# Kernel tuning notes

Measured on AMD Instinct MI355X. Metric: run time of the kernel, lower is better.

The kernel has to match this reference:

```python
import jax, jax.numpy as jnp
import numpy as np

B, N, D, H = 8, 1024, 512, 8
DH = D // H


def setup_inputs() -> dict:
    key = jax.random.key(0)
    ks = jax.random.split(key, 7)
    s = 1.0 / np.sqrt(D)
    return {
        "x": jax.random.normal(ks[0], (B, N, D), dtype=jnp.float32),
        "Wq": jax.random.normal(ks[1], (D, D), dtype=jnp.float32) * s,
        "bq": jax.random.normal(ks[2], (D,), dtype=jnp.float32) * 0.01,
        "Wk": jax.random.normal(ks[3], (D, D), dtype=jnp.float32) * s,
        "bk": jax.random.normal(ks[4], (D,), dtype=jnp.float32) * 0.01,
        "Wv": jax.random.normal(ks[5], (D, D), dtype=jnp.float32) * s,
        "bv": jax.random.normal(ks[6], (D,), dtype=jnp.float32) * 0.01,
    }


def reference(x, Wq, bq, Wk, bk, Wv, bv):
    # Q/K/V projections (nn.Linear: x @ W^T + b; here W stored as [in, out])
    q = x @ Wq + bq  # [B, N, D]
    k = x @ Wk + bk
    v = x @ Wv + bv
    # chunk(dim=2)+cat(dim=0) == split channels into H head groups
    q = q.reshape(B, N, H, DH)
    k = k.reshape(B, N, H, DH)
    v = v.reshape(B, N, H, DH)
    # NOTE: original applies NO 1/sqrt(head_dim) scaling
    scores = jnp.einsum("bqhd,bkhd->bhqk", q, k)  # [B, H, N, N]
    weights = jax.nn.softmax(scores, axis=-1)
    y = jnp.einsum("bhqk,bkhd->bqhd", weights, v)  # [B, N, H, DH]
    return y.reshape(B, N, D)
```

## Files before the change

kernel.cpp:

```cpp
#include <hip/hip_runtime.h>
#include <hip/hip_bf16.h>

typedef _Float16 half8 __attribute__((ext_vector_type(8)));
typedef _Float16 half4v __attribute__((ext_vector_type(4)));
typedef float floatx4 __attribute__((ext_vector_type(4)));

#define BB 8
#define NN 1024
#define DD 512
#define HH 8
#define DHH 64
#define LOG2E 1.4426950408889634f

#define EXP2F(x) __builtin_amdgcn_exp2f(x)

__device__ __forceinline__ void gload_lds16(const _Float16* g, _Float16* l) {
    __builtin_amdgcn_global_load_lds(
        (const __attribute__((address_space(1))) void*)g,
        (__attribute__((address_space(3))) void*)l, 16, 0, 0);
}

__global__ __launch_bounds__(256) void cvt_kernel(const float* __restrict__ Wq,
                                                  const float* __restrict__ Wk,
                                                  const float* __restrict__ Wv,
                                                  _Float16* __restrict__ Wt) {
    __shared__ __align__(16) _Float16 tb[64][72];
    int t = blockIdx.x;
    int tid = threadIdx.x;
    int which = t >> 6;
    int rem = t & 63;
    int kt = (rem >> 3) * 64, nt = (rem & 7) * 64;
    const float* W = (which == 0) ? Wq : (which == 1) ? Wk : Wv;
    float wscale = (which == 0) ? LOG2E : 1.0f;
    _Float16* Wto = Wt + (size_t)which * DD * DD;
    for (int i = 0; i < 16; i++) {
        int idx = tid + i * 256;
        int r = idx >> 6, c = idx & 63;
        tb[c][r] = (_Float16)(W[(size_t)(kt + r) * DD + nt + c] * wscale);
    }
    __syncthreads();
    for (int i = 0; i < 16; i++) {
        int idx = tid + i * 256;
        int r = idx >> 6, c = idx & 63;
        Wto[(size_t)(nt + r) * DD + kt + c] = tb[r][c];
    }
}

__global__ __launch_bounds__(256) void qkv_gemm_kernel(const float* __restrict__ x,
                                                       const _Float16* __restrict__ Wt,
                                                       const float* __restrict__ bq,
                                                       const float* __restrict__ bk,
                                                       const float* __restrict__ bv,
                                                       _Float16* __restrict__ QKV) {
    __shared__ __align__(16) _Float16 Ws[128 * 32];
    __shared__ __align__(16) _Float16 Xs[128 * 32];

    int which = blockIdx.z;
    const _Float16* Wtw = Wt + (size_t)which * DD * DD;
    const float* bias = (which == 0) ? bq : (which == 1) ? bk : bv;
    const float bscale = (which == 0) ? LOG2E : 1.0f;

    int tid = threadIdx.x;
    int wave = tid >> 6, lane = tid & 63;
    int quad = lane >> 4, l16 = lane & 15;
    int wm = wave >> 1, wn = wave & 1;
    int mBase = blockIdx.x * 128;
    int nBase = blockIdx.y * 128;

    int srow = wave * 32 + (lane >> 2);
    int scol = (lane & 3) * 8;
    const _Float16* wg = Wtw + (size_t)(nBase + srow) * DD + scol;
    const float*    xg = x   + (size_t)(mBase + srow) * DD + scol;
    _Float16* wl = Ws + (wave * 32) * 32;

    floatx4 acc[4][4];
    for (int i = 0; i < 4; i++)
        for (int j = 0; j < 4; j++) acc[i][j] = (floatx4){0.f, 0.f, 0.f, 0.f};

    for (int kk = 0; kk < DD; kk += 32) {
        __syncthreads();
        gload_lds16(wg + kk,           wl);
        gload_lds16(wg + 16 * DD + kk, wl + 16 * 32);
        float4 a0 = *(const float4*)(xg + kk);
        float4 a1 = *(const float4*)(xg + kk + 4);
        float4 b0 = *(const float4*)(xg + 16 * DD + kk);
        float4 b1 = *(const float4*)(xg + 16 * DD + kk + 4);
        half8 ha, hb;
        ha[0] = (_Float16)a0.x; ha[1] = (_Float16)a0.y; ha[2] = (_Float16)a0.z; ha[3] = (_Float16)a0.w;
        ha[4] = (_Float16)a1.x; ha[5] = (_Float16)a1.y; ha[6] = (_Float16)a1.z; ha[7] = (_Float16)a1.w;
        hb[0] = (_Float16)b0.x; hb[1] = (_Float16)b0.y; hb[2] = (_Float16)b0.z; hb[3] = (_Float16)b0.w;
        hb[4] = (_Float16)b1.x; hb[5] = (_Float16)b1.y; hb[6] = (_Float16)b1.z; hb[7] = (_Float16)b1.w;
        *(half8*)&Xs[srow * 32 + scol] = ha;
        *(half8*)&Xs[(srow + 16) * 32 + scol] = hb;
        __syncthreads();

        half8 af[4], bf[4];
        if (which < 2) {
            for (int i = 0; i < 4; i++)
                af[i] = *(const half8*)&Ws[(wm * 64 + i * 16 + l16) * 32 + quad * 8];
            for (int j = 0; j < 4; j++)
                bf[j] = *(const half8*)&Xs[(wn * 64 + j * 16 + l16) * 32 + quad * 8];
        } else {
            for (int i = 0; i < 4; i++)
                af[i] = *(const half8*)&Xs[(wm * 64 + i * 16 + l16) * 32 + quad * 8];
            for (int j = 0; j < 4; j++)
                bf[j] = *(const half8*)&Ws[(wn * 64 + j * 16 + l16) * 32 + quad * 8];
        }
        for (int i = 0; i < 4; i++)
            for (int j = 0; j < 4; j++)
                acc[i][j] = __builtin_amdgcn_mfma_f32_16x16x32_f16(af[i], bf[j], acc[i][j], 0, 0, 0);
    }

    if (which < 2) {
        _Float16* out = QKV + (size_t)which * (BB * NN) * DD;
        for (int i = 0; i < 4; i++) {
            int feat0 = nBase + wm * 64 + i * 16 + quad * 4;
            float4 b4 = *(const float4*)&bias[feat0];
            b4.x *= bscale; b4.y *= bscale; b4.z *= bscale; b4.w *= bscale;
            for (int j = 0; j < 4; j++) {
                int token = mBase + wn * 64 + j * 16 + l16;
                half4v pack;
                pack[0] = (_Float16)(acc[i][j][0] + b4.x);
                pack[1] = (_Float16)(acc[i][j][1] + b4.y);
                pack[2] = (_Float16)(acc[i][j][2] + b4.z);
                pack[3] = (_Float16)(acc[i][j][3] + b4.w);
                *(half4v*)&out[(size_t)token * DD + feat0] = pack;
            }
        }
    } else {
        _Float16* VT = QKV + (size_t)2 * (BB * NN) * DD;
        for (int j = 0; j < 4; j++) {
            int col = nBase + wn * 64 + j * 16 + l16;
            float bval = bias[col];
            for (int i = 0; i < 4; i++) {
                int row0 = mBase + wm * 64 + i * 16 + quad * 4;
                int b = row0 >> 10;
                int n = row0 & 1023;
                half4v pack;
                for (int reg = 0; reg < 4; reg++) pack[reg] = (_Float16)(acc[i][j][reg] + bval);
                *(half4v*)&VT[((size_t)b * 512 + col) * 1024 + n] = pack;
            }
        }
    }
}

__device__ __forceinline__ void stage_kv(const _Float16* kg, const _Float16* vg,
                                         _Float16* kl, _Float16* vl, int kt) {
    const _Float16* kgk = kg + (size_t)(kt * 64) * DD;
    const _Float16* vgk = vg + kt * 64;
    gload_lds16(kgk,            kl);
    gload_lds16(kgk + 8 * DD,   kl + 8 * 64);
    gload_lds16(vgk,            vl);
    gload_lds16(vgk + 8 * 1024, vl + 8 * 64);
}

__global__ __launch_bounds__(256) void attn_kernel(const _Float16* __restrict__ QKV,
                                                   float* __restrict__ out) {
    const _Float16* Q  = QKV;
    const _Float16* K  = QKV + (size_t)(BB * NN) * DD;
    const _Float16* VT = QKV + (size_t)2 * (BB * NN) * DD;

    __shared__ __align__(16) _Float16 Kt[2][64 * 64];
    __shared__ __align__(16) _Float16 Vt[2][64 * 64];
    __shared__ __align__(16) _Float16 PT[4][16 * 64];

    int tid = threadIdx.x;
    int wave = tid >> 6, lane = tid & 63;
    int quad = lane >> 4, l16 = lane & 15;
    int l16sw = l16 & 7;
    int bid = blockIdx.x;
    int b = bid & 7;
    int local = bid >> 3;
    int h = local & 7;
    int qt = local >> 3;

    const _Float16* Qb  = Q + ((size_t)b * NN) * DD + h * DHH;
    const _Float16* Kb  = K + ((size_t)b * NN) * DD + h * DHH;
    const _Float16* VTb = VT + ((size_t)b * 512 + h * 64) * 1024;

    int qrow = qt * 64 + wave * 16 + l16;
    half8 qf0 = *(const half8*)(Qb + (size_t)qrow * DD + 0 * 32 + quad * 8);
    half8 qf1 = *(const half8*)(Qb + (size_t)qrow * DD + 1 * 32 + quad * 8);

    floatx4 o[4];
    for (int nt = 0; nt < 4; nt++) o[nt] = (floatx4){0.f, 0.f, 0.f, 0.f};
    float m_i = 0.0f, l_i = 0.f;

    int srow = lane >> 3;
    int schunk = (lane & 7) ^ srow;
    const _Float16* kg = Kb + (size_t)(wave * 16 + srow) * DD + schunk * 8;
    const _Float16* vg = VTb + (size_t)(wave * 16 + srow) * 1024 + schunk * 8;
    _Float16* kl0 = &Kt[0][(wave * 16) * 64];
    _Float16* vl0 = &Vt[0][(wave * 16) * 64];
    _Float16* kl1 = &Kt[1][(wave * 16) * 64];
    _Float16* vl1 = &Vt[1][(wave * 16) * 64];

    stage_kv(kg, vg, kl0, vl0, 0);

    for (int kt = 0; kt < 16; kt++) {
        int cur = kt & 1;
        __syncthreads();
        if (kt + 1 < 16)
            stage_kv(kg, vg, cur ? kl0 : kl1, cur ? vl0 : vl1, kt + 1);

        floatx4 s[4];
        for (int nt = 0; nt < 4; nt++) s[nt] = (floatx4){0.f, 0.f, 0.f, 0.f};
        __builtin_amdgcn_s_setprio(1);
        for (int ks = 0; ks < 2; ks++) {
            half8 qf = ks ? qf1 : qf0;
            for (int nt = 0; nt < 4; nt++) {
                half8 kf = *(const half8*)&Kt[cur][(nt * 16 + l16) * 64
                                                   + (((ks * 4 + quad) ^ l16sw) * 8)];
                s[nt] = __builtin_amdgcn_mfma_f32_16x16x32_f16(kf, qf, s[nt], 0, 0, 0);
            }
        }
        __builtin_amdgcn_s_setprio(0);

        float a0 = fmaxf(fmaxf(s[0][0], s[0][1]), fmaxf(s[0][2], s[0][3]));
        float a1 = fmaxf(fmaxf(s[1][0], s[1][1]), fmaxf(s[1][2], s[1][3]));
        float a2 = fmaxf(fmaxf(s[2][0], s[2][1]), fmaxf(s[2][2], s[2][3]));
        float a3 = fmaxf(fmaxf(s[3][0], s[3][1]), fmaxf(s[3][2], s[3][3]));
        float mx = fmaxf(fmaxf(a0, a1), fmaxf(a2, a3));

        for (int nt = 0; nt < 4; nt++)
            for (int r = 0; r < 4; r++)
                s[nt][r] = EXP2F(s[nt][r] - m_i);
        float r0 = (s[0][0] + s[0][1]) + (s[0][2] + s[0][3]);
        float r1 = (s[1][0] + s[1][1]) + (s[1][2] + s[1][3]);
        float r2 = (s[2][0] + s[2][1]) + (s[2][2] + s[2][3]);
        float r3 = (s[3][0] + s[3][1]) + (s[3][2] + s[3][3]);
        float rs = (r0 + r1) + (r2 + r3);

        float mxs = __shfl_xor(mx, 16, 64);
        float rss = __shfl_xor(rs, 16, 64);
        mx = fmaxf(mx, mxs);
        rs += rss;
        mxs = __shfl_xor(mx, 32, 64);
        rss = __shfl_xor(rs, 32, 64);
        mx = fmaxf(mx, mxs);
        rs += rss;

        if (__any(mx > m_i + 11.5443f)) {
            float mnew = fmaxf(m_i, mx);
            float al = EXP2F(m_i - mnew);
            m_i = mnew;
            l_i *= al;
            rs *= al;
            for (int nt = 0; nt < 4; nt++)
                for (int r = 0; r < 4; r++) {
                    s[nt][r] *= al;
                    o[nt][r] *= al;
                }
        }
        l_i += rs;

        for (int ntl = 0; ntl < 4; ntl++) {
            half4v p4;
            for (int r = 0; r < 4; r++) p4[r] = (_Float16)s[ntl][r];
            *(half4v*)&PT[wave][l16 * 64 + (((ntl * 2 + (quad >> 1)) ^ l16sw) * 8)
                               + (quad & 1) * 4] = p4;
        }

        __builtin_amdgcn_s_setprio(1);
        for (int ks2 = 0; ks2 < 2; ks2++) {
            half8 pf = *(const half8*)&PT[wave][l16 * 64 + (((ks2 * 4 + quad) ^ l16sw) * 8)];
            for (int nt = 0; nt < 4; nt++) {
                half8 vf = *(const half8*)&Vt[cur][(nt * 16 + l16) * 64
                                                   + (((ks2 * 4 + quad) ^ l16sw) * 8)];
                o[nt] = __builtin_amdgcn_mfma_f32_16x16x32_f16(vf, pf, o[nt], 0, 0, 0);
            }
        }
        __builtin_amdgcn_s_setprio(0);
    }

    float inv = 1.0f / l_i;
    float* outb = out + ((size_t)b * NN) * DD + h * DHH;
    int row = qt * 64 + wave * 16 + l16;
    for (int nt = 0; nt < 4; nt++) {
        float4 st;
        st.x = o[nt][0] * inv; st.y = o[nt][1] * inv;
        st.z = o[nt][2] * inv; st.w = o[nt][3] * inv;
        *(float4*)&outb[(size_t)row * DD + nt * 16 + quad * 4] = st;
    }
}

extern "C" void kernel_launch(void* const* d_in, const int* in_sizes, int n_in,
                              void* d_out, int out_size, void* d_ws, size_t ws_size,
                              hipStream_t stream) {
    const float* x  = (const float*)d_in[0];
    const float* Wq = (const float*)d_in[1];
    const float* bq = (const float*)d_in[2];
    const float* Wk = (const float*)d_in[3];
    const float* bk = (const float*)d_in[4];
    const float* Wv = (const float*)d_in[5];
    const float* bv = (const float*)d_in[6];
    float* out = (float*)d_out;

    _Float16* Wt  = (_Float16*)d_ws;
    _Float16* QKV = Wt + (size_t)3 * DD * DD;

    hipLaunchKernelGGL(cvt_kernel, dim3(192), dim3(256), 0, stream,
                       Wq, Wk, Wv, Wt);
    hipLaunchKernelGGL(qkv_gemm_kernel, dim3(64, 4, 3), dim3(256), 0, stream,
                       x, Wt, bq, bk, bv, QKV);
    hipLaunchKernelGGL(attn_kernel, dim3(1024), dim3(256), 0, stream, QKV, out);
}
```

Before: 136.1 us.

## Process two query sub-tiles per wave to reuse K/V fragments

New measurement: 139.8 us. 1.03x slower.

```diff
diff --git a/kernel.cpp b/kernel.cpp
--- a/kernel.cpp
+++ b/kernel.cpp
@@ -3,6 +3,7 @@
 
 typedef _Float16 half8 __attribute__((ext_vector_type(8)));
 typedef _Float16 half4v __attribute__((ext_vector_type(4)));
+typedef __fp16 fp16x2 __attribute__((ext_vector_type(2)));
 typedef float floatx4 __attribute__((ext_vector_type(4)));
 
 #define BB 8
@@ -162,7 +163,7 @@
 
     __shared__ __align__(16) _Float16 Kt[2][64 * 64];
     __shared__ __align__(16) _Float16 Vt[2][64 * 64];
-    __shared__ __align__(16) _Float16 PT[4][16 * 64];
+    __shared__ __align__(16) _Float16 PT[4][2][16 * 64];
 
     int tid = threadIdx.x;
     int wave = tid >> 6, lane = tid & 63;
@@ -178,13 +179,16 @@
     const _Float16* Kb  = K + ((size_t)b * NN) * DD + h * DHH;
     const _Float16* VTb = VT + ((size_t)b * 512 + h * 64) * 1024;
 
-    int qrow = qt * 64 + wave * 16 + l16;
-    half8 qf0 = *(const half8*)(Qb + (size_t)qrow * DD + 0 * 32 + quad * 8);
-    half8 qf1 = *(const half8*)(Qb + (size_t)qrow * DD + 1 * 32 + quad * 8);
-
-    floatx4 o[4];
-    for (int nt = 0; nt < 4; nt++) o[nt] = (floatx4){0.f, 0.f, 0.f, 0.f};
-    float m_i = 0.0f, l_i = 0.f;
+    int qrow0 = qt * 128 + wave * 32 + l16;
+    half8 qf[2][2];
+    for (int g = 0; g < 2; g++)
+        for (int ks = 0; ks < 2; ks++)
+            qf[g][ks] = *(const half8*)(Qb + (size_t)(qrow0 + g * 16) * DD + ks * 32 + quad * 8);
+
+    floatx4 o[4][2];
+    for (int nt = 0; nt < 4; nt++)
+        for (int g = 0; g < 2; g++) o[nt][g] = (floatx4){0.f, 0.f, 0.f, 0.f};
+    float m0 = 0.f, m1 = 0.f, l0 = 0.f, l1 = 0.f;
 
     int srow = lane >> 3;
     int schunk = (lane & 7) ^ srow;
@@ -195,92 +199,128 @@
     _Float16* kl1 = &Kt[1][(wave * 16) * 64];
     _Float16* vl1 = &Vt[1][(wave * 16) * 64];
 
+    int kidx0 = l16 * 64 + (((0 * 4 + quad) ^ l16sw) * 8);
+    int kidx1 = l16 * 64 + (((1 * 4 + quad) ^ l16sw) * 8);
+    int pw0 = l16 * 64 + (((0 + (quad >> 1)) ^ l16sw) * 8) + (quad & 1) * 4;
+    int pw1 = l16 * 64 + (((2 + (quad >> 1)) ^ l16sw) * 8) + (quad & 1) * 4;
+    int pw2 = l16 * 64 + (((4 + (quad >> 1)) ^ l16sw) * 8) + (quad & 1) * 4;
+    int pw3 = l16 * 64 + (((6 + (quad >> 1)) ^ l16sw) * 8) + (quad & 1) * 4;
+
     stage_kv(kg, vg, kl0, vl0, 0);
 
-    for (int kt = 0; kt < 16; kt++) {
-        int cur = kt & 1;
+    auto tilebody = [&](int kt, int cur) {
         __syncthreads();
         if (kt + 1 < 16)
             stage_kv(kg, vg, cur ? kl0 : kl1, cur ? vl0 : vl1, kt + 1);
 
-        floatx4 s[4];
-        for (int nt = 0; nt < 4; nt++) s[nt] = (floatx4){0.f, 0.f, 0.f, 0.f};
+        floatx4 s[4][2];
+        for (int nt = 0; nt < 4; nt++)
+            for (int g = 0; g < 2; g++) s[nt][g] = (floatx4){0.f, 0.f, 0.f, 0.f};
         __builtin_amdgcn_s_setprio(1);
         for (int ks = 0; ks < 2; ks++) {
-            half8 qf = ks ? qf1 : qf0;
+            int kb = ks ? kidx1 : kidx0;
             for (int nt = 0; nt < 4; nt++) {
-                half8 kf = *(const half8*)&Kt[cur][(nt * 16 + l16) * 64
-                                                   + (((ks * 4 + quad) ^ l16sw) * 8)];
-                s[nt] = __builtin_amdgcn_mfma_f32_16x16x32_f16(kf, qf, s[nt], 0, 0, 0);
+                half8 kf = *(const half8*)&Kt[cur][kb + nt * 1024];
+                s[nt][0] = __builtin_amdgcn_mfma_f32_16x16x32_f16(kf, qf[0][ks], s[nt][0], 0, 0, 0);
+                s[nt][1] = __builtin_amdgcn_mfma_f32_16x16x32_f16(kf, qf[1][ks], s[nt][1], 0, 0, 0);
             }
         }
         __builtin_amdgcn_s_setprio(0);
 
-        float a0 = fmaxf(fmaxf(s[0][0], s[0][1]), fmaxf(s[0][2], s[0][3]));
-        float a1 = fmaxf(fmaxf(s[1][0], s[1][1]), fmaxf(s[1][2], s[1][3]));
-        float a2 = fmaxf(fmaxf(s[2][0], s[2][1]), fmaxf(s[2][2], s[2][3]));
-        float a3 = fmaxf(fmaxf(s[3][0], s[3][1]), fmaxf(s[3][2], s[3][3]));
-        float mx = fmaxf(fmaxf(a0, a1), fmaxf(a2, a3));
+        float ax0 = fmaxf(fmaxf(s[0][0][0], s[0][0][1]), fmaxf(s[0][0][2], s[0][0][3]));
+        float ax1 = fmaxf(fmaxf(s[1][0][0], s[1][0][1]), fmaxf(s[1][0][2], s[1][0][3]));
+        float ax2 = fmaxf(fmaxf(s[2][0][0], s[2][0][1]), fmaxf(s[2][0][2], s[2][0][3]));
+        float ax3 = fmaxf(fmaxf(s[3][0][0], s[3][0][1]), fmaxf(s[3][0][2], s[3][0][3]));
+        float bx0 = fmaxf(fmaxf(s[0][1][0], s[0][1][1]), fmaxf(s[0][1][2], s[0][1][3]));
+        float bx1 = fmaxf(fmaxf(s[1][1][0], s[1][1][1]), fmaxf(s[1][1][2], s[1][1][3]));
+        float bx2 = fmaxf(fmaxf(s[2][1][0], s[2][1][1]), fmaxf(s[2][1][2], s[2][1][3]));
+        float bx3 = fmaxf(fmaxf(s[3][1][0], s[3][1][1]), fmaxf(s[3][1][2], s[3][1][3]));
+        float mx0 = fmaxf(fmaxf(ax0, ax1), fmaxf(ax2, ax3));
+        float mx1 = fmaxf(fmaxf(bx0, bx1), fmaxf(bx2, bx3));
 
         for (int nt = 0; nt < 4; nt++)
-            for (int r = 0; r < 4; r++)
-                s[nt][r] = EXP2F(s[nt][r] - m_i);
-        float r0 = (s[0][0] + s[0][1]) + (s[0][2] + s[0][3]);
-        float r1 = (s[1][0] + s[1][1]) + (s[1][2] + s[1][3]);
-        float r2 = (s[2][0] + s[2][1]) + (s[2][2] + s[2][3]);
-        float r3 = (s[3][0] + s[3][1]) + (s[3][2] + s[3][3]);
-        float rs = (r0 + r1) + (r2 + r3);
-
-        float mxs = __shfl_xor(mx, 16, 64);
-        float rss = __shfl_xor(rs, 16, 64);
-        mx = fmaxf(mx, mxs);
-        rs += rss;
-        mxs = __shfl_xor(mx, 32, 64);
-        rss = __shfl_xor(rs, 32, 64);
-        mx = fmaxf(mx, mxs);
-        rs += rss;
-
-        if (__any(mx > m_i + 11.5443f)) {
-            float mnew = fmaxf(m_i, mx);
-            float al = EXP2F(m_i - mnew);
-            m_i = mnew;
-            l_i *= al;
-            rs *= al;
+            for (int r = 0; r < 4; r++) {
+                s[nt][0][r] = EXP2F(s[nt][0][r] - m0);
+                s[nt][1][r] = EXP2F(s[nt][1][r] - m1);
+            }
+        float ra0 = (s[0][0][0] + s[0][0][1]) + (s[0][0][2] + s[0][0][3]);
+        float ra1 = (s[1][0][0] + s[1][0][1]) + (s[1][0][2] + s[1][0][3]);
+        float ra2 = (s[2][0][0] + s[2][0][1]) + (s[2][0][2] + s[2][0][3]);
+        float ra3 = (s[3][0][0] + s[3][0][1]) + (s[3][0][2] + s[3][0][3]);
+        float rb0 = (s[0][1][0] + s[0][1][1]) + (s[0][1][2] + s[0][1][3]);
+        float rb1 = (s[1][1][0] + s[1][1][1]) + (s[1][1][2] + s[1][1][3]);
+        float rb2 = (s[2][1][0] + s[2][1][1]) + (s[2][1][2] + s[2][1][3]);
+        float rb3 = (s[3][1][0] + s[3][1][1]) + (s[3][1][2] + s[3][1][3]);
+        float rs0 = (ra0 + ra1) + (ra2 + ra3);
+        float rs1 = (rb0 + rb1) + (rb2 + rb3);
+
+        float t0 = __shfl_xor(mx0, 16, 64);
+        float t1 = __shfl_xor(mx1, 16, 64);
+        float t2 = __shfl_xor(rs0, 16, 64);
+        float t3 = __shfl_xor(rs1, 16, 64);
+        mx0 = fmaxf(mx0, t0); mx1 = fmaxf(mx1, t1); rs0 += t2; rs1 += t3;
+        t0 = __shfl_xor(mx0, 32, 64);
+        t1 = __shfl_xor(mx1, 32, 64);
+        t2 = __shfl_xor(rs0, 32, 64);
+        t3 = __shfl_xor(rs1, 32, 64);
+        mx0 = fmaxf(mx0, t0); mx1 = fmaxf(mx1, t1); rs0 += t2; rs1 += t3;
+
+        if (__any(fmaxf(mx0 - m0, mx1 - m1) > 11.5443f)) {
+            float mn0 = fmaxf(m0, mx0), mn1 = fmaxf(m1, mx1);
+            float al0 = EXP2F(m0 - mn0), al1 = EXP2F(m1 - mn1);
+            m0 = mn0; m1 = mn1;
+            l0 *= al0; l1 *= al1;
+            rs0 *= al0; rs1 *= al1;
             for (int nt = 0; nt < 4; nt++)
                 for (int r = 0; r < 4; r++) {
-                    s[nt][r] *= al;
-                    o[nt][r] *= al;
+                    s[nt][0][r] *= al0; o[nt][0][r] *= al0;
+                    s[nt][1][r] *= al1; o[nt][1][r] *= al1;
                 }
         }
-        l_i += rs;
-
-        for (int ntl = 0; ntl < 4; ntl++) {
-            half4v p4;
-            for (int r = 0; r < 4; r++) p4[r] = (_Float16)s[ntl][r];
-            *(half4v*)&PT[wave][l16 * 64 + (((ntl * 2 + (quad >> 1)) ^ l16sw) * 8)
-                               + (quad & 1) * 4] = p4;
+        l0 += rs0; l1 += rs1;
+
+        for (int g = 0; g < 2; g++) {
+            int pw[4] = {pw0, pw1, pw2, pw3};
+            for (int ntl = 0; ntl < 4; ntl++) {
+                fp16x2 lo = __builtin_amdgcn_cvt_pkrtz(s[ntl][g][0], s[ntl][g][1]);
+                fp16x2 hi = __builtin_amdgcn_cvt_pkrtz(s[ntl][g][2], s[ntl][g][3]);
+                half4v p4;
+                p4[0] = (_Float16)lo[0]; p4[1] = (_Float16)lo[1];
+                p4[2] = (_Float16)hi[0]; p4[3] = (_Float16)hi[1];
+                *(half4v*)&PT[wave][g][pw[ntl]] = p4;
+            }
         }
 
         __builtin_amdgcn_s_setprio(1);
         for (int ks2 = 0; ks2 < 2; ks2++) {
-            half8 pf = *(const half8*)&PT[wave][l16 * 64 + (((ks2 * 4 + quad) ^ l16sw) * 8)];
+            int kb = ks2 ? kidx1 : kidx0;
+            half8 pf0 = *(const half8*)&PT[wave][0][kb];
+            half8 pf1 = *(const half8*)&PT[wave][1][kb];
             for (int nt = 0; nt < 4; nt++) {
-                half8 vf = *(const half8*)&Vt[cur][(nt * 16 + l16) * 64
-                                                   + (((ks2 * 4 + quad) ^ l16sw) * 8)];
-                o[nt] = __builtin_amdgcn_mfma_f32_16x16x32_f16(vf, pf, o[nt], 0, 0, 0);
+                half8 vf = *(const half8*)&Vt[cur][kb + nt * 1024];
+                o[nt][0] = __builtin_amdgcn_mfma_f32_16x16x32_f16(vf, pf0, o[nt][0], 0, 0, 0);
+                o[nt][1] = __builtin_amdgcn_mfma_f32_16x16x32_f16(vf, pf1, o[nt][1], 0, 0, 0);
             }
         }
         __builtin_amdgcn_s_setprio(0);
-    }
-
-    float inv = 1.0f / l_i;
+    };
+
+    for (int kt2 = 0; kt2 < 8; kt2++) {
+        tilebody(2 * kt2, 0);
+        tilebody(2 * kt2 + 1, 1);
+    }
+
+    float inv0 = 1.0f / l0, inv1 = 1.0f / l1;
     float* outb = out + ((size_t)b * NN) * DD + h * DHH;
-    int row = qt * 64 + wave * 16 + l16;
-    for (int nt = 0; nt < 4; nt++) {
-        float4 st;
-        st.x = o[nt][0] * inv; st.y = o[nt][1] * inv;
-        st.z = o[nt][2] * inv; st.w = o[nt][3] * inv;
-        *(float4*)&outb[(size_t)row * DD + nt * 16 + quad * 4] = st;
+    for (int g = 0; g < 2; g++) {
+        int row = qt * 128 + wave * 32 + g * 16 + l16;
+        float inv = g ? inv1 : inv0;
+        for (int nt = 0; nt < 4; nt++) {
+            float4 st;
+            st.x = o[nt][g][0] * inv; st.y = o[nt][g][1] * inv;
+            st.z = o[nt][g][2] * inv; st.w = o[nt][g][3] * inv;
+            *(float4*)&outb[(size_t)row * DD + nt * 16 + quad * 4] = st;
+        }
     }
 }
 
@@ -303,5 +343,5 @@
                        Wq, Wk, Wv, Wt);
     hipLaunchKernelGGL(qkv_gemm_kernel, dim3(64, 4, 3), dim3(256), 0, stream,
                        x, Wt, bq, bk, bv, QKV);
-    hipLaunchKernelGGL(attn_kernel, dim3(1024), dim3(256), 0, stream, QKV, out);
-}
+    hipLaunchKernelGGL(attn_kernel, dim3(512), dim3(256), 0, stream, QKV, out);
+}
```

## Double QKV GEMM K-tile to 64 with XOR-swizzled LDS layout

Applied to the files above, without the earlier changes.

Result: slower. 142.1 us (+4.4%).

```diff
diff --git a/kernel.cpp b/kernel.cpp
--- a/kernel.cpp
+++ b/kernel.cpp
@@ -52,8 +52,8 @@
                                                        const float* __restrict__ bk,
                                                        const float* __restrict__ bv,
                                                        _Float16* __restrict__ QKV) {
-    __shared__ __align__(16) _Float16 Ws[128 * 32];
-    __shared__ __align__(16) _Float16 Xs[128 * 32];
+    __shared__ __align__(16) _Float16 Ws[128 * 64];
+    __shared__ __align__(16) _Float16 Xs[128 * 64];
 
     int which = blockIdx.z;
     const _Float16* Wtw = Wt + (size_t)which * DD * DD;
@@ -63,52 +63,66 @@
     int tid = threadIdx.x;
     int wave = tid >> 6, lane = tid & 63;
     int quad = lane >> 4, l16 = lane & 15;
+    int l16sw = l16 & 7;
     int wm = wave >> 1, wn = wave & 1;
     int mBase = blockIdx.x * 128;
     int nBase = blockIdx.y * 128;
 
-    int srow = wave * 32 + (lane >> 2);
-    int scol = (lane & 3) * 8;
-    const _Float16* wg = Wtw + (size_t)(nBase + srow) * DD + scol;
-    const float*    xg = x   + (size_t)(mBase + srow) * DD + scol;
-    _Float16* wl = Ws + (wave * 32) * 32;
+    int wrow7 = lane >> 3;
+    int wchunk = (lane & 7) ^ wrow7;
+    const _Float16* wg = Wtw + (size_t)(nBase + wave * 32 + wrow7) * DD + wchunk * 8;
+    _Float16* wl = Ws + (wave * 32) * 64;
+
+    int sxrow = wave * 32 + (lane >> 2);
+    int sxr7 = (lane >> 2) & 7;
+    const float* xg = x + (size_t)(mBase + sxrow) * DD + (lane & 3) * 8;
 
     floatx4 acc[4][4];
     for (int i = 0; i < 4; i++)
         for (int j = 0; j < 4; j++) acc[i][j] = (floatx4){0.f, 0.f, 0.f, 0.f};
 
-    for (int kk = 0; kk < DD; kk += 32) {
+    for (int kk = 0; kk < DD; kk += 64) {
         __syncthreads();
-        gload_lds16(wg + kk,           wl);
-        gload_lds16(wg + 16 * DD + kk, wl + 16 * 32);
-        float4 a0 = *(const float4*)(xg + kk);
-        float4 a1 = *(const float4*)(xg + kk + 4);
-        float4 b0 = *(const float4*)(xg + 16 * DD + kk);
-        float4 b1 = *(const float4*)(xg + 16 * DD + kk + 4);
-        half8 ha, hb;
-        ha[0] = (_Float16)a0.x; ha[1] = (_Float16)a0.y; ha[2] = (_Float16)a0.z; ha[3] = (_Float16)a0.w;
-        ha[4] = (_Float16)a1.x; ha[5] = (_Float16)a1.y; ha[6] = (_Float16)a1.z; ha[7] = (_Float16)a1.w;
-        hb[0] = (_Float16)b0.x; hb[1] = (_Float16)b0.y; hb[2] = (_Float16)b0.z; hb[3] = (_Float16)b0.w;
-        hb[4] = (_Float16)b1.x; hb[5] = (_Float16)b1.y; hb[6] = (_Float16)b1.z; hb[7] = (_Float16)b1.w;
-        *(half8*)&Xs[srow * 32 + scol] = ha;
-        *(half8*)&Xs[(srow + 16) * 32 + scol] = hb;
+        for (int j = 0; j < 4; j++)
+            gload_lds16(wg + (size_t)(j * 8) * DD + kk, wl + (j * 8) * 64);
+        for (int rg = 0; rg < 2; rg++) {
+            int row = sxrow + rg * 16;
+            const float* xr = xg + (size_t)(rg * 16) * DD + kk;
+            for (int kh = 0; kh < 2; kh++) {
+                float4 a0 = *(const float4*)(xr + kh * 32);
+                float4 a1 = *(const float4*)(xr + kh * 32 + 4);
+                half8 ha;
+                ha[0] = (_Float16)a0.x; ha[1] = (_Float16)a0.y;
+                ha[2] = (_Float16)a0.z; ha[3] = (_Float16)a0.w;
+                ha[4] = (_Float16)a1.x; ha[5] = (_Float16)a1.y;
+                ha[6] = (_Float16)a1.z; ha[7] = (_Float16)a1.w;
+                int chunk = (kh * 4 + (lane & 3)) ^ sxr7;
+                *(half8*)&Xs[row * 64 + chunk * 8] = ha;
+            }
+        }
         __syncthreads();
 
-        half8 af[4], bf[4];
-        if (which < 2) {
+        for (int ks = 0; ks < 2; ks++) {
+            half8 af[4], bf[4];
+            if (which < 2) {
+                for (int i = 0; i < 4; i++)
+                    af[i] = *(const half8*)&Ws[(wm * 64 + i * 16 + l16) * 64
+                                               + (((ks * 4 + quad) ^ l16sw) * 8)];
+                for (int j = 0; j < 4; j++)
+                    bf[j] = *(const half8*)&Xs[(wn * 64 + j * 16 + l16) * 64
+                                               + (((ks * 4 + quad) ^ l16sw) * 8)];
+            } else {
+                for (int i = 0; i < 4; i++)
+                    af[i] = *(const half8*)&Xs[(wm * 64 + i * 16 + l16) * 64
+                                               + (((ks * 4 + quad) ^ l16sw) * 8)];
+                for (int j = 0; j < 4; j++)
+                    bf[j] = *(const half8*)&Ws[(wn * 64 + j * 16 + l16) * 64
+                                               + (((ks * 4 + quad) ^ l16sw) * 8)];
+            }
             for (int i = 0; i < 4; i++)
-                af[i] = *(const half8*)&Ws[(wm * 64 + i * 16 + l16) * 32 + quad * 8];
-            for (int j = 0; j < 4; j++)
-                bf[j] = *(const half8*)&Xs[(wn * 64 + j * 16 + l16) * 32 + quad * 8];
-        } else {
-            for (int i = 0; i < 4; i++)
-                af[i] = *(const half8*)&Xs[(wm * 64 + i * 16 + l16) * 32 + quad * 8];
-            for (int j = 0; j < 4; j++)
-                bf[j] = *(const half8*)&Ws[(wn * 64 + j * 16 + l16) * 32 + quad * 8];
-        }
-        for (int i = 0; i < 4; i++)
-            for (int j = 0; j < 4; j++)
-                acc[i][j] = __builtin_amdgcn_mfma_f32_16x16x32_f16(af[i], bf[j], acc[i][j], 0, 0, 0);
+                for (int j = 0; j < 4; j++)
+                    acc[i][j] = __builtin_amdgcn_mfma_f32_16x16x32_f16(af[i], bf[j], acc[i][j], 0, 0, 0);
+        }
     }
 
     if (which < 2) {
```

## Load K and V fragments directly from global memory, dropping LDS staging

Applied to the files above, without the earlier changes.

Measured after the change: 217.9 us. +60.1%, slower.

```diff
diff --git a/kernel.cpp b/kernel.cpp
--- a/kernel.cpp
+++ b/kernel.cpp
@@ -144,24 +144,12 @@
     }
 }
 
-__device__ __forceinline__ void stage_kv(const _Float16* kg, const _Float16* vg,
-                                         _Float16* kl, _Float16* vl, int kt) {
-    const _Float16* kgk = kg + (size_t)(kt * 64) * DD;
-    const _Float16* vgk = vg + kt * 64;
-    gload_lds16(kgk,            kl);
-    gload_lds16(kgk + 8 * DD,   kl + 8 * 64);
-    gload_lds16(vgk,            vl);
-    gload_lds16(vgk + 8 * 1024, vl + 8 * 64);
-}
-
 __global__ __launch_bounds__(256) void attn_kernel(const _Float16* __restrict__ QKV,
                                                    float* __restrict__ out) {
     const _Float16* Q  = QKV;
     const _Float16* K  = QKV + (size_t)(BB * NN) * DD;
     const _Float16* VT = QKV + (size_t)2 * (BB * NN) * DD;
 
-    __shared__ __align__(16) _Float16 Kt[2][64 * 64];
-    __shared__ __align__(16) _Float16 Vt[2][64 * 64];
     __shared__ __align__(16) _Float16 PT[4][16 * 64];
 
     int tid = threadIdx.x;
@@ -186,31 +174,17 @@
     for (int nt = 0; nt < 4; nt++) o[nt] = (floatx4){0.f, 0.f, 0.f, 0.f};
     float m_i = 0.0f, l_i = 0.f;
 
-    int srow = lane >> 3;
-    int schunk = (lane & 7) ^ srow;
-    const _Float16* kg = Kb + (size_t)(wave * 16 + srow) * DD + schunk * 8;
-    const _Float16* vg = VTb + (size_t)(wave * 16 + srow) * 1024 + schunk * 8;
-    _Float16* kl0 = &Kt[0][(wave * 16) * 64];
-    _Float16* vl0 = &Vt[0][(wave * 16) * 64];
-    _Float16* kl1 = &Kt[1][(wave * 16) * 64];
-    _Float16* vl1 = &Vt[1][(wave * 16) * 64];
-
-    stage_kv(kg, vg, kl0, vl0, 0);
+    const _Float16* kgl = Kb + (size_t)l16 * DD + quad * 8;
+    const _Float16* vgl = VTb + (size_t)l16 * 1024 + quad * 8;
 
     for (int kt = 0; kt < 16; kt++) {
-        int cur = kt & 1;
-        __syncthreads();
-        if (kt + 1 < 16)
-            stage_kv(kg, vg, cur ? kl0 : kl1, cur ? vl0 : vl1, kt + 1);
-
         floatx4 s[4];
         for (int nt = 0; nt < 4; nt++) s[nt] = (floatx4){0.f, 0.f, 0.f, 0.f};
         __builtin_amdgcn_s_setprio(1);
         for (int ks = 0; ks < 2; ks++) {
             half8 qf = ks ? qf1 : qf0;
             for (int nt = 0; nt < 4; nt++) {
-                half8 kf = *(const half8*)&Kt[cur][(nt * 16 + l16) * 64
-                                                   + (((ks * 4 + quad) ^ l16sw) * 8)];
+                half8 kf = *(const half8*)(kgl + (size_t)(kt * 64 + nt * 16) * DD + ks * 32);
                 s[nt] = __builtin_amdgcn_mfma_f32_16x16x32_f16(kf, qf, s[nt], 0, 0, 0);
             }
         }
@@ -265,8 +239,7 @@
         for (int ks2 = 0; ks2 < 2; ks2++) {
             half8 pf = *(const half8*)&PT[wave][l16 * 64 + (((ks2 * 4 + quad) ^ l16sw) * 8)];
             for (int nt = 0; nt < 4; nt++) {
-                half8 vf = *(const half8*)&Vt[cur][(nt * 16 + l16) * 64
-                                                   + (((ks2 * 4 + quad) ^ l16sw) * 8)];
+                half8 vf = *(const half8*)(vgl + (size_t)(nt * 16) * 1024 + kt * 64 + ks2 * 32);
                 o[nt] = __builtin_amdgcn_mfma_f32_16x16x32_f16(vf, pf, o[nt], 0, 0, 0);
             }
         }
```
